# Performance work log

Hardware: AMD Instinct MI355X
Metric: run time of the kernel (lower is better)

The kernel has to match this reference:

```python
import jax, jax.numpy as jnp
import numpy as np
from jax import lax

T = 4          # num_steps
TAU = 2.0      # spikingjelly LIFNode default tau
VTH = 1.0      # v_threshold
ALPHA = 2.0    # ATan surrogate default alpha
EPS = 1e-5     # BatchNorm eps

@jax.custom_vjp
def atan_spike(x):
    # Heaviside forward, ATan surrogate backward (spikingjelly surrogate.ATan)
    return (x >= 0.0).astype(x.dtype)

def _atan_fwd(x):
    return atan_spike(x), x

def _atan_bwd(x, g):
    sg = (ALPHA / 2.0) / (1.0 + (jnp.pi / 2.0 * ALPHA * x) ** 2)
    return (g * sg,)

atan_spike.defvjp(_atan_fwd, _atan_bwd)

def lif_multistep(x_seq):
    # x_seq: (T, B, D, L). LIF with decay_input=True, v_reset=0.0, hard reset,
    # detach_reset=True (reset spike is stop-gradiented).
    def step(v, xt):
        h = v + (xt - v) / TAU          # membrane charge
        s = atan_spike(h - VTH)          # spike
        v_new = h * (1.0 - lax.stop_gradient(s))  # hard reset to 0
        return v_new, s
    _, spikes = lax.scan(step, jnp.zeros_like(x_seq[0]), x_seq)
    return spikes  # (T, B, D, L)

def setup_inputs() -> dict:
    key = jax.random.key(0)
    k1, k2, k3, k4 = jax.random.split(key, 4)
    L, TB, D = 2048, 128, 128
    x = jax.random.normal(k1, (L, TB, D), dtype=jnp.float32)
    conv_w = jax.random.normal(k2, (D, D, 3), dtype=jnp.float32) * 0.05
    bn_gamma = jnp.ones((D,), jnp.float32)
    bn_beta = jnp.zeros((D,), jnp.float32)
    bn_mean = jax.random.normal(k3, (D,), dtype=jnp.float32) * 0.1
    bn_var = jax.random.uniform(k4, (D,), dtype=jnp.float32, minval=0.5, maxval=1.5)
    return {"x": x, "conv_w": conv_w, "bn_gamma": bn_gamma, "bn_beta": bn_beta,
            "bn_mean": bn_mean, "bn_var": bn_var}

def reference(x, conv_w, bn_gamma, bn_beta, bn_mean, bn_var):
    # x: (L, TB, D)
    L, TB, D = x.shape
    xf = jnp.transpose(x, (1, 2, 0))  # (TB, D, L)
    # Conv1d(D, D, k=3, stride=1, pad=1, bias=False)
    xf = lax.conv_general_dilated(xf, conv_w, window_strides=(1,),
                                  padding=((1, 1),),
                                  dimension_numbers=("NCH", "OIH", "NCH"))
    # BatchNorm1d in inference mode (running stats)
    scale = bn_gamma * lax.rsqrt(bn_var + EPS)
    xf = (xf - bn_mean[None, :, None]) * scale[None, :, None] + bn_beta[None, :, None]
    # (TB, D, L) -> (T, B, D, L), multi-step LIF
    xs = xf.reshape(T, TB // T, D, L)
    sp = lif_multistep(xs)
    sp = sp.reshape(TB, D, L)   # flatten(0, 1); dropout is identity in eval
    return x + jnp.transpose(sp, (2, 0, 1))  # (L, TB, D)
```

## Files before the change

kernel.cpp:

```cpp
#include <hip/hip_runtime.h>


constexpr int L   = 2048;
constexpr int NTB = 128;
constexpr int D   = 128;
constexpr int T   = 4;
constexpr int LT  = 64;
constexpr int NP  = LT + 2;
constexpr int JT  = 8;

__global__ __launch_bounds__(256, 3)
void snn_conv_lif(const float* __restrict__ x, const float* __restrict__ w,
                  const float* __restrict__ gamma, const float* __restrict__ beta,
                  const float* __restrict__ mean, const float* __restrict__ var,
                  float* __restrict__ out) {
    __shared__ float xs[NP * D];
    __shared__ float ws[24 * 32 * 4];

    const int tid = threadIdx.x;
    const int b   = blockIdx.x & 31;
    const int lt  = blockIdx.x >> 5;
    const int l0  = lt * LT;
    const int q4  = tid & 31;
    const int p0  = (tid >> 6) * 16 + ((tid >> 5) & 1) * JT;

    float sc[4], bi[4];
    {
        const float4 g4 = ((const float4*)gamma)[q4];
        const float4 b4 = ((const float4*)beta)[q4];
        const float4 m4 = ((const float4*)mean)[q4];
        const float4 v4 = ((const float4*)var)[q4];
        const float gg[4] = {g4.x, g4.y, g4.z, g4.w};
        const float bb[4] = {b4.x, b4.y, b4.z, b4.w};
        const float mm[4] = {m4.x, m4.y, m4.z, m4.w};
        const float vv[4] = {v4.x, v4.y, v4.z, v4.w};
        #pragma unroll
        for (int oo = 0; oo < 4; ++oo) {
            sc[oo] = gg[oo] / sqrtf(vv[oo] + 1e-5f);
            bi[oo] = bb[oo] - mm[oo] * sc[oo];
        }
    }

    float v[4][JT];
    #pragma unroll
    for (int oo = 0; oo < 4; ++oo)
        #pragma unroll
        for (int j = 0; j < JT; ++j) v[oo][j] = 0.f;

    #pragma unroll 1
    for (int t = 0; t < T; ++t) {
        const int n = t * 32 + b;
        __syncthreads();
        for (int idx = tid; idx < NP * 32; idx += 256) {
            const int p = idx >> 5, c = idx & 31;
            const int l = l0 - 1 + p;
            float4 val = make_float4(0.f, 0.f, 0.f, 0.f);
            if (l >= 0 && l < L)
                val = ((const float4*)x)[(l * NTB + n) * (D / 4) + c];
            ((float4*)xs)[p * (D / 4) + c] = val;
        }

        float a[4][JT];
        #pragma unroll
        for (int oo = 0; oo < 4; ++oo)
            #pragma unroll
            for (int j = 0; j < JT; ++j) a[oo][j] = 0.f;

        #pragma unroll 1
        for (int it = 0; it < 16; ++it) {
            __syncthreads();
            #pragma unroll
            for (int r = 0; r < 3; ++r) {
                const int idx = tid + r * 256;
                const int qq  = idx & 31;
                const int cc  = idx >> 5;
                const int f   = cc >> 2;
                const int oo  = cc & 3;
                const float4 wv = *((const float4*)(w + (4 * qq + oo) * (D * 3) + it * 24 + f * 4));
                *((float4*)(ws + ((oo * 6 + f) * 32 + qq) * 4)) = wv;
            }
            __syncthreads();

            #pragma unroll
            for (int i4 = 0; i4 < 2; ++i4) {
                float4 W0[4], W1[4], W2[4];
                #pragma unroll
                for (int oo = 0; oo < 4; ++oo) {
                    const float* wp = ws + ((oo * 6 + i4 * 3) * 32 + q4) * 4;
                    W0[oo] = *((const float4*)(wp));
                    W1[oo] = *((const float4*)(wp + 128));
                    W2[oo] = *((const float4*)(wp + 256));
                }

                const int ii = it * 2 + i4;
                const float4* xcol = (const float4*)xs + ii;
                float4 xa = xcol[(p0 + 0) * 32];
                float4 xb = xcol[(p0 + 1) * 32];
                #pragma unroll
                for (int j = 0; j < JT; ++j) {
                    const float4 xc = xcol[(p0 + j + 2) * 32];
                    #pragma unroll
                    for (int oo = 0; oo < 4; ++oo) {
                        float s = a[oo][j];
                        const float4 w0 = W0[oo], w1 = W1[oo], w2 = W2[oo];
                        s = fmaf(xa.x, w0.x, s);
                        s = fmaf(xa.y, w0.w, s);
                        s = fmaf(xa.z, w1.z, s);
                        s = fmaf(xa.w, w2.y, s);
                        s = fmaf(xb.x, w0.y, s);
                        s = fmaf(xb.y, w1.x, s);
                        s = fmaf(xb.z, w1.w, s);
                        s = fmaf(xb.w, w2.z, s);
                        s = fmaf(xc.x, w0.z, s);
                        s = fmaf(xc.y, w1.y, s);
                        s = fmaf(xc.z, w2.x, s);
                        s = fmaf(xc.w, w2.w, s);
                        a[oo][j] = s;
                    }
                    xa = xb; xb = xc;
                }
            }
        }

        #pragma unroll
        for (int j = 0; j < JT; ++j) {
            const float4 res = ((const float4*)xs)[(p0 + j + 1) * 32 + q4];
            const float rr[4] = {res.x, res.y, res.z, res.w};
            float ov[4];
            #pragma unroll
            for (int oo = 0; oo < 4; ++oo) {
                const float y = fmaf(a[oo][j], sc[oo], bi[oo]);
                const float h = 0.5f * (v[oo][j] + y);
                const bool fire = (h >= 1.0f);
                v[oo][j] = fire ? 0.0f : h;
                ov[oo] = rr[oo] + (fire ? 1.0f : 0.0f);
            }
            const int l = l0 + p0 + j;
            ((float4*)out)[(l * NTB + n) * 32 + q4] =
                make_float4(ov[0], ov[1], ov[2], ov[3]);
        }
    }
}

extern "C" void kernel_launch(void* const* d_in, const int* in_sizes, int n_in,
                              void* d_out, int out_size, void* d_ws, size_t ws_size,
                              hipStream_t stream) {
    const float* x     = (const float*)d_in[0];
    const float* w     = (const float*)d_in[1];
    const float* gamma = (const float*)d_in[2];
    const float* beta  = (const float*)d_in[3];
    const float* mean  = (const float*)d_in[4];
    const float* var   = (const float*)d_in[5];
    float* out = (float*)d_out;

    dim3 grid((L / LT) * 32);
    dim3 block(256);
    snn_conv_lif<<<grid, block, 0, stream>>>(x, w, gamma, beta, mean, var, out);
}
```

Baseline: 578.9 us.

## Pre-transpose conv weights and register-prefetch next weight chunk during compute

Adds a small pre-kernel that rearranges the conv weights into the exact per-chunk layout the main kernel stores in shared memory, so each staging step becomes contiguous float4 loads. The main loop now loads the next chunk into registers before computing the current one, then writes it to shared memory afterwards, hiding global load latency behind the FMA work. In exchange it adds an extra kernel launch, uses the workspace buffer, and raises register pressure with three extra float4 values under a 3-blocks-per-SM launch bound.

```diff
diff --git a/kernel.cpp b/kernel.cpp
--- a/kernel.cpp
+++ b/kernel.cpp
@@ -9,13 +9,26 @@
 constexpr int NP  = LT + 2;
 constexpr int JT  = 8;
 
+__global__ void transpose_w(const float* __restrict__ w, float* __restrict__ wt) {
+    const int i = blockIdx.x * 256 + threadIdx.x;
+    if (i >= 16 * 768) return;
+    const int it = i / 768;
+    const int d  = i - it * 768;
+    const int qq = d & 31;
+    const int m  = d >> 5;
+    const int oo = m / 6;
+    const int f  = m - 6 * oo;
+    const float4 val = *((const float4*)(w + (4 * qq + oo) * (D * 3) + it * 24 + f * 4));
+    ((float4*)wt)[i] = val;
+}
+
 __global__ __launch_bounds__(256, 3)
-void snn_conv_lif(const float* __restrict__ x, const float* __restrict__ w,
+void snn_conv_lif(const float* __restrict__ x, const float* __restrict__ wt,
                   const float* __restrict__ gamma, const float* __restrict__ beta,
                   const float* __restrict__ mean, const float* __restrict__ var,
                   float* __restrict__ out) {
     __shared__ float xs[NP * D];
-    __shared__ float ws[24 * 32 * 4];
+    __shared__ float ws[768 * 4];
 
     const int tid = threadIdx.x;
     const int b   = blockIdx.x & 31;
@@ -23,6 +36,7 @@
     const int l0  = lt * LT;
     const int q4  = tid & 31;
     const int p0  = (tid >> 6) * 16 + ((tid >> 5) & 1) * JT;
+    const float4* wt4 = (const float4*)wt;
 
     float sc[4], bi[4];
     {
@@ -50,6 +64,11 @@
     #pragma unroll 1
     for (int t = 0; t < T; ++t) {
         const int n = t * 32 + b;
+
+        float4 wp[3];
+        #pragma unroll
+        for (int r = 0; r < 3; ++r) wp[r] = wt4[tid + r * 256];
+
         __syncthreads();
         for (int idx = tid; idx < NP * 32; idx += 256) {
             const int p = idx >> 5, c = idx & 31;
@@ -59,6 +78,9 @@
                 val = ((const float4*)x)[(l * NTB + n) * (D / 4) + c];
             ((float4*)xs)[p * (D / 4) + c] = val;
         }
+        #pragma unroll
+        for (int r = 0; r < 3; ++r) ((float4*)ws)[tid + r * 256] = wp[r];
+        __syncthreads();
 
         float a[4][JT];
         #pragma unroll
@@ -68,28 +90,21 @@
 
         #pragma unroll 1
         for (int it = 0; it < 16; ++it) {
-            __syncthreads();
-            #pragma unroll
-            for (int r = 0; r < 3; ++r) {
-                const int idx = tid + r * 256;
-                const int qq  = idx & 31;
-                const int cc  = idx >> 5;
-                const int f   = cc >> 2;
-                const int oo  = cc & 3;
-                const float4 wv = *((const float4*)(w + (4 * qq + oo) * (D * 3) + it * 24 + f * 4));
-                *((float4*)(ws + ((oo * 6 + f) * 32 + qq) * 4)) = wv;
+            if (it < 15) {
+                #pragma unroll
+                for (int r = 0; r < 3; ++r)
+                    wp[r] = wt4[(it + 1) * 768 + tid + r * 256];
             }
-            __syncthreads();
 
             #pragma unroll
             for (int i4 = 0; i4 < 2; ++i4) {
                 float4 W0[4], W1[4], W2[4];
                 #pragma unroll
                 for (int oo = 0; oo < 4; ++oo) {
-                    const float* wp = ws + ((oo * 6 + i4 * 3) * 32 + q4) * 4;
-                    W0[oo] = *((const float4*)(wp));
-                    W1[oo] = *((const float4*)(wp + 128));
-                    W2[oo] = *((const float4*)(wp + 256));
+                    const float* wpt = ws + ((oo * 6 + i4 * 3) * 32 + q4) * 4;
+                    W0[oo] = *((const float4*)(wpt));
+                    W1[oo] = *((const float4*)(wpt + 128));
+                    W2[oo] = *((const float4*)(wpt + 256));
                 }
 
                 const int ii = it * 2 + i4;
@@ -119,6 +134,13 @@
                     }
                     xa = xb; xb = xc;
                 }
+            }
+
+            if (it < 15) {
+                __syncthreads();
+                #pragma unroll
+                for (int r = 0; r < 3; ++r) ((float4*)ws)[tid + r * 256] = wp[r];
+                __syncthreads();
             }
         }
 
@@ -152,8 +174,11 @@
     const float* mean  = (const float*)d_in[4];
     const float* var   = (const float*)d_in[5];
     float* out = (float*)d_out;
+    float* wt  = (float*)d_ws;
+
+    transpose_w<<<dim3(48), dim3(256), 0, stream>>>(w, wt);
 
     dim3 grid((L / LT) * 32);
     dim3 block(256);
-    snn_conv_lif<<<grid, block, 0, stream>>>(x, w, gamma, beta, mean, var, out);
+    snn_conv_lif<<<grid, block, 0, stream>>>(x, wt, gamma, beta, mean, var, out);
 }
```

After: 2.150 ms. +271.3%, slower.
